# Optimization experiments

Hardware: AMD Instinct MI355X
Metric: run time of the kernel (lower is better)

Reference implementation:

```python
import jax, jax.numpy as jnp
import numpy as np

N_NODES = 100000
IN_DIM = 128
HID_DIM = 128
N_EDGES = 1600000
BN_EPS = 1e-5


def setup_inputs() -> dict:
    key = jax.random.key(0)
    k1, k2, k3, k4 = jax.random.split(key, 4)
    x = jax.random.normal(k1, (N_NODES, IN_DIM), dtype=jnp.float32)
    edge_index = jax.random.randint(k2, (2, N_EDGES), 0, N_NODES, dtype=jnp.int64)
    # GCNConv linear weight (glorot) and bias
    W = jax.random.normal(k3, (HID_DIM, IN_DIM), dtype=jnp.float32) * (1.0 / np.sqrt(IN_DIM))
    b = jnp.zeros((HID_DIM,), dtype=jnp.float32)
    # BatchNorm affine params
    gamma = jnp.ones((HID_DIM,), dtype=jnp.float32)
    beta = jnp.zeros((HID_DIM,), dtype=jnp.float32)
    return {"x": x, "edge_index": edge_index, "W": W, "b": b, "gamma": gamma, "beta": beta}


def reference(x, edge_index, W, b, gamma, beta):
    n = x.shape[0]
    # --- GCNConv: add self loops, symmetric normalization ---
    loops = jnp.arange(n, dtype=edge_index.dtype)
    row = jnp.concatenate([edge_index[0], loops])  # source j
    col = jnp.concatenate([edge_index[1], loops])  # target i
    deg = jax.ops.segment_sum(jnp.ones_like(col, dtype=x.dtype), col, num_segments=n)
    deg_inv_sqrt = jnp.where(deg > 0, jax.lax.rsqrt(jnp.maximum(deg, 1e-12)), 0.0)
    norm = deg_inv_sqrt[row] * deg_inv_sqrt[col]  # [E+N]
    # linear transform then normalized gather-scatter aggregation
    h = x @ W.T  # [N, H]
    msgs = h[row] * norm[:, None]  # [E+N, H]
    out = jax.ops.segment_sum(msgs, col, num_segments=n) + b  # [N, H]
    # --- BatchNorm1d (training-mode batch stats, biased var) + ReLU ---
    mean = jnp.mean(out, axis=0)
    var = jnp.mean(jnp.square(out - mean), axis=0)
    out = (out - mean) * jax.lax.rsqrt(var + BN_EPS) * gamma + beta
    return jax.nn.relu(out)
```

## Files before the change

### kernel.cpp

```cpp
#include <hip/hip_runtime.h>

#define N_NODES 100000
#define N_EDGES 1600000
#define BN_EPS 1e-5f
#define SB 25
#define SCAP 69632
#define NBB 800
#define CAP 2688

typedef short short8 __attribute__((ext_vector_type(8)));
typedef float floatx4 __attribute__((ext_vector_type(4)));

__device__ __forceinline__ unsigned short f2bf(float f) {
    unsigned int u = __float_as_uint(f);
    unsigned int r = (u + 0x7fffu + ((u >> 16) & 1u)) >> 16;
    return (unsigned short)r;
}
__device__ __forceinline__ float bflo(unsigned int v) { return __uint_as_float(v << 16); }
__device__ __forceinline__ float bfhi(unsigned int v) { return __uint_as_float(v & 0xffff0000u); }

__global__ __launch_bounds__(512) void k_binA(const int* __restrict__ ei,
                                              int* __restrict__ scnt,
                                              unsigned int* __restrict__ b1, int E) {
    __shared__ int hist[32], base[32], gbase[32];
    __shared__ unsigned int stage[4096];
    __shared__ unsigned char stb[4096];
    int tid = threadIdx.x;
    int e0 = blockIdx.x * 4096;
    int cn = min(4096, E - e0);
    if (tid < 32) hist[tid] = 0;
    __syncthreads();

    unsigned int mycode[8];
    short myslot[8];
    signed char myb[8];
    #pragma unroll
    for (int j = 0; j < 8; j++) {
        int idx = j * 512 + tid;
        if (idx < cn) {
            int src = ei[e0 + idx];
            int dst = ei[E + e0 + idx];
            int s = dst >> 12;
            mycode[j] = (unsigned int)src | ((unsigned int)(dst & 4095) << 17);
            myb[j] = (signed char)s;
            myslot[j] = (short)atomicAdd(&hist[s], 1);
        } else myb[j] = -1;
    }
    __syncthreads();
    if (tid == 0) {
        int run = 0;
        for (int s = 0; s < SB; s++) { base[s] = run; run += hist[s]; }
    }
    __syncthreads();
    #pragma unroll
    for (int j = 0; j < 8; j++) {
        if (myb[j] >= 0) {
            int p = base[myb[j]] + myslot[j];
            stage[p] = mycode[j];
            stb[p] = (unsigned char)myb[j];
        }
    }
    if (tid < SB && hist[tid]) gbase[tid] = tid * SCAP + atomicAdd(&scnt[tid], hist[tid]);
    __syncthreads();
    for (int i = tid; i < cn; i += 512) {
        int s = stb[i];
        b1[gbase[s] + (i - base[s])] = stage[i];
    }
}

__global__ __launch_bounds__(512) void k_binB(const unsigned int* __restrict__ b1,
                                              const int* __restrict__ scnt,
                                              int* __restrict__ bcnt,
                                              unsigned int* __restrict__ b2) {
    __shared__ int hist[32], base[32], gbase[32];
    __shared__ unsigned int stage[4096];
    __shared__ unsigned char stb[4096];
    int tid = threadIdx.x;
    int s = blockIdx.x / 17;
    int c = blockIdx.x % 17;
    int cnt = scnt[s];
    int e0 = s * SCAP + c * 4096;
    int cn = min(4096, cnt - c * 4096);
    if (tid < 32) hist[tid] = 0;
    __syncthreads();

    unsigned int mycode[8];
    short myslot[8];
    signed char myb[8];
    #pragma unroll
    for (int j = 0; j < 8; j++) {
        int idx = j * 512 + tid;
        if (idx < cn) {
            unsigned int code = b1[e0 + idx];
            int sub = (code >> 24) & 31;
            mycode[j] = code & 0x00FFFFFFu;
            myb[j] = (signed char)sub;
            myslot[j] = (short)atomicAdd(&hist[sub], 1);
        } else myb[j] = -1;
    }
    __syncthreads();
    if (tid == 0) {
        int run = 0;
        for (int k = 0; k < 32; k++) { base[k] = run; run += hist[k]; }
    }
    __syncthreads();
    #pragma unroll
    for (int j = 0; j < 8; j++) {
        if (myb[j] >= 0) {
            int p = base[myb[j]] + myslot[j];
            stage[p] = mycode[j];
            stb[p] = (unsigned char)myb[j];
        }
    }
    if (tid < 32 && hist[tid]) {
        int gb = s * 32 + tid;
        gbase[tid] = gb * CAP + atomicAdd(&bcnt[gb], hist[tid]);
    }
    __syncthreads();
    for (int i = tid; i < cn; i += 512) {
        int sub = stb[i];
        b2[gbase[sub] + (i - base[sub])] = stage[i];
    }
}

__global__ __launch_bounds__(256) void k_dd(const unsigned int* __restrict__ binned,
                                            const int* __restrict__ bcnt,
                                            float* __restrict__ dinv, int n) {
    __shared__ int hist[128];
    int b = blockIdx.x, t = threadIdx.x;
    int nb0 = b * 128;
    int e0 = b * CAP;
    int cnt = bcnt[b];
    if (t < 128) hist[t] = 0;
    __syncthreads();
    for (int i = t; i < cnt; i += 256)
        atomicAdd(&hist[binned[e0 + i] >> 17], 1);
    __syncthreads();
    int nr = min(128, n - nb0);
    if (t < nr) dinv[nb0 + t] = rsqrtf((float)(hist[t] + 1));
}

__global__ void k_wcvt(const float* __restrict__ Wf, unsigned short* __restrict__ Wb) {
    int i = blockIdx.x * 256 + threadIdx.x;
    if (i < 128 * 128) Wb[i] = f2bf(Wf[i]);
}

__global__ __launch_bounds__(256) void k_gemm(const float* __restrict__ x,
                                              const unsigned short* __restrict__ Wb,
                                              const float* __restrict__ dinv,
                                              unsigned short* __restrict__ gb, int n) {
    int w = threadIdx.x >> 6;
    int l = threadIdx.x & 63;
    int rowbase = blockIdx.x * 128 + w * 32;
    int r16 = l & 15;
    int kg = l >> 4;

    short8 a[2][4];
    float dv[2][4];
    #pragma unroll
    for (int m = 0; m < 2; m++) {
        int row = rowbase + m * 16 + r16;
        int rca = min(row, n - 1);
        const float* base = x + rca * 128;
        #pragma unroll
        for (int q = 0; q < 4; q++) {
            const float4* xp = (const float4*)(base + q * 32 + kg * 8);
            float4 lo = xp[0], hi = xp[1];
            short8 af;
            af[0] = (short)f2bf(lo.x); af[1] = (short)f2bf(lo.y);
            af[2] = (short)f2bf(lo.z); af[3] = (short)f2bf(lo.w);
            af[4] = (short)f2bf(hi.x); af[5] = (short)f2bf(hi.y);
            af[6] = (short)f2bf(hi.z); af[7] = (short)f2bf(hi.w);
            a[m][q] = af;
        }
        #pragma unroll
        for (int r = 0; r < 4; r++)
            dv[m][r] = dinv[min(rowbase + m * 16 + kg * 4 + r, n - 1)];
    }
    for (int t = 0; t < 8; t++) {
        int col = t * 16 + r16;
        short8 b[4];
        #pragma unroll
        for (int q = 0; q < 4; q++)
            b[q] = *(const short8*)(Wb + col * 128 + q * 32 + kg * 8);

        floatx4 acc[2] = {};
        #pragma unroll
        for (int m = 0; m < 2; m++)
            #pragma unroll
            for (int q = 0; q < 4; q++)
                acc[m] = __builtin_amdgcn_mfma_f32_16x16x32_bf16(a[m][q], b[q], acc[m], 0, 0, 0);

        #pragma unroll
        for (int m = 0; m < 2; m++) {
            #pragma unroll
            for (int r = 0; r < 4; r++) {
                int row = rowbase + m * 16 + kg * 4 + r;
                if (row < n) gb[row * 128 + col] = f2bf(acc[m][r] * dv[m][r]);
            }
        }
    }
}

__global__ __launch_bounds__(512) void k_fused(const unsigned int* __restrict__ hp,
        const float* __restrict__ dinv, const int* __restrict__ bcnt,
        const unsigned int* __restrict__ binned, float* __restrict__ out,
        float* __restrict__ sums, float* __restrict__ sumsq, int n) {
    __shared__ int hist[128], hsc[128];
    __shared__ float dl[128];
    __shared__ unsigned int sh_src[CAP];
    __shared__ float ps[8][128], pq[8][128];
    int t = threadIdx.x;
    int w = t >> 6, l = t & 63;
    int b = blockIdx.x;
    int nb0 = b * 128;
    int e0 = b * CAP;
    int cnt = bcnt[b];
    int nr = min(128, n - nb0);

    if (t < 128) {
        hist[t] = 0;
        if (t < nr) dl[t] = dinv[nb0 + t];
    }
    __syncthreads();

    unsigned int mycode[6];
    short myslot[6];
    #pragma unroll
    for (int j = 0; j < 6; j++) {
        int i = j * 512 + t;
        if (i < cnt) {
            unsigned int code = binned[e0 + i];
            mycode[j] = code;
            myslot[j] = (short)atomicAdd(&hist[code >> 17], 1);
        } else myslot[j] = -1;
    }
    __syncthreads();

    int v = (t < 128) ? hist[t] : 0;
    if (t < 128) hsc[t] = v;
    __syncthreads();
    for (int o = 1; o < 128; o <<= 1) {
        int x = (t < 128 && t >= o) ? hsc[t - o] : 0;
        __syncthreads();
        if (t < 128) hsc[t] += x;
        __syncthreads();
    }

    #pragma unroll
    for (int j = 0; j < 6; j++) {
        if (myslot[j] >= 0) {
            unsigned int code = mycode[j];
            int ld = code >> 17;
            int pos = hsc[ld] - hist[ld] + myslot[j];
            sh_src[pos] = code & 0x1FFFF;
        }
    }
    __syncthreads();

    float s0 = 0, s1 = 0, q0 = 0, q1 = 0;
    for (int r = w; r < nr; r += 8) {
        int i = nb0 + r;
        float di = dl[r];
        unsigned int sv = hp[i * 64 + l];
        float ax = bflo(sv);
        float ay = bfhi(sv);
        int off = hsc[r] - hist[r];
        int dg = hist[r];
        int e = 0;
        for (; e + 15 < dg; e += 16) {
            unsigned int hv[16];
            #pragma unroll
            for (int j = 0; j < 16; j++)
                hv[j] = hp[sh_src[off + e + j] * 64 + l];
            #pragma unroll
            for (int j = 0; j < 16; j++) {
                ax += bflo(hv[j]);
                ay += bfhi(hv[j]);
            }
        }
        for (; e + 3 < dg; e += 4) {
            unsigned int hv[4];
            #pragma unroll
            for (int j = 0; j < 4; j++)
                hv[j] = hp[sh_src[off + e + j] * 64 + l];
            #pragma unroll
            for (int j = 0; j < 4; j++) {
                ax += bflo(hv[j]);
                ay += bfhi(hv[j]);
            }
        }
        for (; e < dg; e++) {
            unsigned int hv = hp[sh_src[off + e] * 64 + l];
            ax += bflo(hv);
            ay += bfhi(hv);
        }
        float v0 = di * ax, v1 = di * ay;
        ((float2*)out)[i * 64 + l] = make_float2(v0, v1);
        s0 += v0; q0 += v0 * v0;
        s1 += v1; q1 += v1 * v1;
    }

    ps[w][2 * l] = s0; ps[w][2 * l + 1] = s1;
    pq[w][2 * l] = q0; pq[w][2 * l + 1] = q1;
    __syncthreads();
    if (t < 128) {
        float s = 0, q = 0;
        #pragma unroll
        for (int j = 0; j < 8; j++) { s += ps[j][t]; q += pq[j][t]; }
        atomicAdd(&sums[t], s);
        atomicAdd(&sumsq[t], q);
    }
}

__global__ void k_bn(float* __restrict__ out, const float* __restrict__ sums,
                     const float* __restrict__ sumsq, const float* __restrict__ gamma,
                     const float* __restrict__ beta, int n) {
    int idx = blockIdx.x * 256 + threadIdx.x;
    int total = n * 32;
    if (idx >= total) return;
    int c0 = (idx & 31) * 4;
    float invN = 1.0f / (float)n;
    float4 v = ((const float4*)out)[idx];
    float r[4] = {v.x, v.y, v.z, v.w};
    #pragma unroll
    for (int j = 0; j < 4; j++) {
        int c = c0 + j;
        float mean = sums[c] * invN;
        float var = sumsq[c] * invN - mean * mean;
        float scale = rsqrtf(var + BN_EPS) * gamma[c];
        float o = (r[j] - mean) * scale + beta[c];
        r[j] = fmaxf(o, 0.0f);
    }
    ((float4*)out)[idx] = make_float4(r[0], r[1], r[2], r[3]);
}

extern "C" void kernel_launch(void* const* d_in, const int* in_sizes, int n_in,
                              void* d_out, int out_size, void* d_ws, size_t ws_size,
                              hipStream_t stream) {
    const float* x     = (const float*)d_in[0];
    const int*   ei    = (const int*)d_in[1];
    const float* W     = (const float*)d_in[2];
    const float* gamma = (const float*)d_in[4];
    const float* beta  = (const float*)d_in[5];
    float* out = (float*)d_out;

    const int n = N_NODES, E = N_EDGES;

    unsigned short* gbuf = (unsigned short*)d_ws;
    float* dinv   = (float*)(gbuf + 12800000);
    float* sums   = dinv + 100000;
    float* sumsq  = sums + 128;
    int*   bcnt   = (int*)(sumsq + 128);
    int*   scnt   = bcnt + NBB;
    unsigned short* Wb = (unsigned short*)(scnt + SB);
    unsigned int* b1 = (unsigned int*)(Wb + 16384);
    unsigned int* b2 = b1 + SB * SCAP;

    hipMemsetAsync(sums, 0, (256 + NBB + SB) * sizeof(int), stream);

    k_binA<<<(E + 4095) / 4096, 512, 0, stream>>>(ei, scnt, b1, E);
    k_binB<<<SB * 17, 512, 0, stream>>>(b1, scnt, bcnt, b2);
    k_dd<<<NBB, 256, 0, stream>>>(b2, bcnt, dinv, n);

    k_wcvt<<<64, 256, 0, stream>>>(W, Wb);
    k_gemm<<<(n + 127) / 128, 256, 0, stream>>>(x, Wb, dinv, gbuf, n);

    k_fused<<<NBB, 512, 0, stream>>>((const unsigned int*)gbuf, dinv, bcnt, b2,
                                     out, sums, sumsq, n);

    k_bn<<<(n * 32 + 255) / 256, 256, 0, stream>>>(out, sums, sumsq, gamma, beta, n);
}
```

Measured before the change: 159.6 us.

## Split aggregation into two channel halves per block with edge-parallel half-waves

Launches two blocks per 128-node bucket, each covering 64 of the 128 channels. Within a wave, the two 32-lane halves handle alternating edges and combine their partial sums with a cross-half shuffle. The aim is more blocks and more independent gathers in flight, which raises memory-level parallelism for the latency-bound neighbour gather. In exchange, each block repeats the bucket's counting and sorting of edges in shared memory, and each gather becomes a 128-byte row segment instead of a full 256-byte row.

```diff
diff --git a/kernel.cpp b/kernel.cpp
--- a/kernel.cpp
+++ b/kernel.cpp
@@ -209,10 +209,14 @@
     __shared__ int hist[128], hsc[128];
     __shared__ float dl[128];
     __shared__ unsigned int sh_src[CAP];
-    __shared__ float ps[8][128], pq[8][128];
+    __shared__ float ps[8][64], pq[8][64];
     int t = threadIdx.x;
     int w = t >> 6, l = t & 63;
-    int b = blockIdx.x;
+    int bid = blockIdx.x;
+    int b = bid >> 1;
+    int ch = bid & 1;
+    int half = l >> 5;
+    int cu = ch * 32 + (l & 31);
     int nb0 = b * 128;
     int e0 = b * CAP;
     int cnt = bcnt[b];
@@ -262,54 +266,58 @@
     for (int r = w; r < nr; r += 8) {
         int i = nb0 + r;
         float di = dl[r];
-        unsigned int sv = hp[i * 64 + l];
-        float ax = bflo(sv);
-        float ay = bfhi(sv);
+        float ax = 0.f, ay = 0.f;
         int off = hsc[r] - hist[r];
         int dg = hist[r];
         int e = 0;
         for (; e + 15 < dg; e += 16) {
-            unsigned int hv[16];
+            unsigned int hv[8];
             #pragma unroll
-            for (int j = 0; j < 16; j++)
-                hv[j] = hp[sh_src[off + e + j] * 64 + l];
+            for (int j = 0; j < 8; j++)
+                hv[j] = hp[sh_src[off + e + 2 * j + half] * 64 + cu];
             #pragma unroll
-            for (int j = 0; j < 16; j++) {
+            for (int j = 0; j < 8; j++) {
                 ax += bflo(hv[j]);
                 ay += bfhi(hv[j]);
             }
         }
         for (; e + 3 < dg; e += 4) {
-            unsigned int hv[4];
-            #pragma unroll
-            for (int j = 0; j < 4; j++)
-                hv[j] = hp[sh_src[off + e + j] * 64 + l];
-            #pragma unroll
-            for (int j = 0; j < 4; j++) {
-                ax += bflo(hv[j]);
-                ay += bfhi(hv[j]);
+            unsigned int h0 = hp[sh_src[off + e + half] * 64 + cu];
+            unsigned int h1 = hp[sh_src[off + e + 2 + half] * 64 + cu];
+            ax += bflo(h0) + bflo(h1);
+            ay += bfhi(h0) + bfhi(h1);
+        }
+        for (; e < dg; e += 2) {
+            int idx = e + half;
+            if (idx < dg) {
+                unsigned int hv = hp[sh_src[off + idx] * 64 + cu];
+                ax += bflo(hv);
+                ay += bfhi(hv);
             }
         }
-        for (; e < dg; e++) {
-            unsigned int hv = hp[sh_src[off + e] * 64 + l];
-            ax += bflo(hv);
-            ay += bfhi(hv);
-        }
-        float v0 = di * ax, v1 = di * ay;
-        ((float2*)out)[i * 64 + l] = make_float2(v0, v1);
-        s0 += v0; q0 += v0 * v0;
-        s1 += v1; q1 += v1 * v1;
-    }
-
-    ps[w][2 * l] = s0; ps[w][2 * l + 1] = s1;
-    pq[w][2 * l] = q0; pq[w][2 * l + 1] = q1;
-    __syncthreads();
-    if (t < 128) {
+        ax += __shfl_xor(ax, 32);
+        ay += __shfl_xor(ay, 32);
+        if (half == 0) {
+            unsigned int sv = hp[i * 64 + cu];
+            float v0 = di * (ax + bflo(sv));
+            float v1 = di * (ay + bfhi(sv));
+            ((float2*)out)[i * 64 + cu] = make_float2(v0, v1);
+            s0 += v0; q0 += v0 * v0;
+            s1 += v1; q1 += v1 * v1;
+        }
+    }
+
+    if (half == 0) {
+        ps[w][2 * (l & 31)] = s0; ps[w][2 * (l & 31) + 1] = s1;
+        pq[w][2 * (l & 31)] = q0; pq[w][2 * (l & 31) + 1] = q1;
+    }
+    __syncthreads();
+    if (t < 64) {
         float s = 0, q = 0;
         #pragma unroll
         for (int j = 0; j < 8; j++) { s += ps[j][t]; q += pq[j][t]; }
-        atomicAdd(&sums[t], s);
-        atomicAdd(&sumsq[t], q);
+        atomicAdd(&sums[ch * 64 + t], s);
+        atomicAdd(&sumsq[ch * 64 + t], q);
     }
 }
 
@@ -366,8 +374,8 @@
     k_wcvt<<<64, 256, 0, stream>>>(W, Wb);
     k_gemm<<<(n + 127) / 128, 256, 0, stream>>>(x, Wb, dinv, gbuf, n);
 
-    k_fused<<<NBB, 512, 0, stream>>>((const unsigned int*)gbuf, dinv, bcnt, b2,
-                                     out, sums, sumsq, n);
+    k_fused<<<NBB * 2, 512, 0, stream>>>((const unsigned int*)gbuf, dinv, bcnt, b2,
+                                         out, sums, sumsq, n);
 
     k_bn<<<(n * 32 + 255) / 256, 256, 0, stream>>>(out, sums, sumsq, gamma, beta, n);
 }
```

After: 162.7 us. About the same (+1.9%).
